# Optimization experiments

Measured on AMD Instinct MI355X. Metric: run time of the kernel, lower is better.

## Reference

```python
import jax, jax.numpy as jnp
import numpy as np

N = 8192      # input_shape[0]: side of the square complex weights A, B
UNITS = 33    # cell units; x has UNITS-1 features, state z has UNITS


def setup_inputs() -> dict:
    key = jax.random.key(0)
    ks = jax.random.split(key, 8)
    s = np.float32(1.0 / np.sqrt(N))  # keep tanh pre-activations O(1)
    f32 = jnp.float32
    return {
        "x_re": jax.random.normal(ks[0], (N, UNITS - 1), f32),
        "x_im": jax.random.normal(ks[1], (N, UNITS - 1), f32),
        "z_re": jax.random.normal(ks[2], (N, UNITS), f32),
        "z_im": jax.random.normal(ks[3], (N, UNITS), f32),
        "A_re": jax.random.normal(ks[4], (N, N), f32) * s,
        "A_im": jax.random.normal(ks[5], (N, N), f32) * s,
        "B_re": jax.random.normal(ks[6], (N, N), f32) * s,
        "B_im": jax.random.normal(ks[7], (N, N), f32) * s,
    }


def reference(x_re, x_im, z_re, z_im, A_re, A_im, B_re, B_im):
    # Assemble complex64 operands (TF cell stores A, B as complex64).
    x = jax.lax.complex(x_re, x_im)          # [N, UNITS-1]
    z = jax.lax.complex(z_re, z_im)          # [N, UNITS]
    A = jax.lax.complex(A_re, A_im)          # [N, N]
    B = jax.lax.complex(B_re, B_im)          # [N, N]

    z_0 = z[:, 0:1]                          # carried-through first column
    z_n = z[:, 1:]                           # [N, UNITS-1]

    # y_t = tanh(A @ z_n + B @ x)  (complex tanh, as tf.keras tanh on complex64)
    y_t = jnp.tanh(jnp.matmul(A, z_n) + jnp.matmul(B, x))

    # new state / output: concat([z_0, y_t], -1) -> [N, UNITS]
    return jnp.concatenate([z_0, y_t], axis=-1)
```

## Files before the change

### kernel.cpp

```cpp
#include <hip/hip_runtime.h>

#define NN 8192
#define UNITS 33
#define NCOLS 32
#define NSTEPS 512
#define NCHUNKB 8
#define CHUNKK (NN / NCHUNKB)
#define TILEK 128
#define TPC (CHUNKK / TILEK)
#define NSLAB (NCHUNKB * 4)

#define RPB 16
#define KT 32
#define NT (NN / KT)
#define SA_STRIDE 20
#define SZ_STRIDE 36
#define SA_MAT (KT * SA_STRIDE)
#define SZ_SRC (KT * SZ_STRIDE)
#define SA_FLOATS (4 * SA_MAT)
#define SZ_BASE SA_FLOATS
#define SH_FLOATS (SA_FLOATS + 4 * SZ_SRC)

typedef __attribute__((ext_vector_type(2)))  float f32x2;
typedef __attribute__((ext_vector_type(4)))  float f32x4;
typedef __attribute__((ext_vector_type(16))) float f32x16;
typedef __attribute__((ext_vector_type(8)))  short bf16x8;
typedef __attribute__((ext_vector_type(4)))  unsigned int u32x4;

union FragU { u32x4 u; bf16x8 s; };

#define MFMA(a, b, c) __builtin_amdgcn_mfma_f32_32x32x16_bf16(a, b, c, 0, 0, 0)

__device__ __forceinline__ float bfr(float v) {
    unsigned int u = __builtin_bit_cast(unsigned int, v);
    u = (u + 0x7FFFu + ((u >> 16) & 1u)) & 0xFFFF0000u;
    return __builtin_bit_cast(float, u);
}

__device__ __forceinline__ void split1(float v, unsigned int &h, unsigned int &l) {
    unsigned int u = __builtin_bit_cast(unsigned int, v);
    unsigned int hu = u >> 16;
    float hf = __builtin_bit_cast(float, hu << 16);
    float r = v - hf;
    unsigned int ru = __builtin_bit_cast(unsigned int, r);
    h = hu;
    l = (ru + 0x8000u) >> 16;
}

__device__ __forceinline__ void packHL(const unsigned int* h, const unsigned int* l,
                                       bf16x8 &hi, bf16x8 &lo) {
    FragU H, L;
    H.u.x = h[0] | (h[1] << 16); H.u.y = h[2] | (h[3] << 16);
    H.u.z = h[4] | (h[5] << 16); H.u.w = h[6] | (h[7] << 16);
    L.u.x = l[0] | (l[1] << 16); L.u.y = l[2] | (l[3] << 16);
    L.u.z = l[4] | (l[5] << 16); L.u.w = l[6] | (l[7] << 16);
    hi = H.s; lo = L.s;
}

__device__ __forceinline__ void mk_split(f32x4 a0, f32x4 a1, bf16x8 &hi, bf16x8 &lo) {
    unsigned int h[8], l[8];
#pragma unroll
    for (int e = 0; e < 4; ++e) { split1(a0[e], h[e], l[e]); split1(a1[e], h[e + 4], l[e + 4]); }
    packHL(h, l, hi, lo);
}

__device__ __forceinline__ bf16x8 fneg(bf16x8 f) {
    FragU x; x.s = f;
    x.u.x ^= 0x80008000u; x.u.y ^= 0x80008000u; x.u.z ^= 0x80008000u; x.u.w ^= 0x80008000u;
    return x.s;
}

__device__ __forceinline__ void probe_cd(int lane, int pm[16], int pn[16]) {
    int m = lane & 31, half = lane >> 5;
    unsigned int am, dummy;
    split1((float)m, am, dummy);
    unsigned int a1; split1(1.0f, a1, dummy);
    unsigned int bn; split1((float)(64 * m), bn, dummy);
    unsigned int av = (half == 0) ? am : a1;
    unsigned int bv = (half == 0) ? a1 : bn;
    FragU A, B;
    A.u.x = A.u.y = A.u.z = A.u.w = av | (av << 16);
    B.u.x = B.u.y = B.u.z = B.u.w = bv | (bv << 16);
    f32x16 d = {};
    d = MFMA(A.s, B.s, d);
#pragma unroll
    for (int r = 0; r < 16; ++r) {
        unsigned int u = (unsigned int)(d[r] * 0.125f + 0.5f);
        pm[r] = (int)(u & 63u);
        pn[r] = (int)(u >> 6);
    }
}

__device__ __forceinline__ void ctanhd(float af, float bf, float &re, float &im) {
    double a = (double)af, b = (double)bf;
    double e  = exp(2.0 * a);
    double ei = 1.0 / e;
    double ch = 0.5 * (e + ei);
    double sh = 0.5 * (e - ei);
    double cb = cos(2.0 * b);
    double sb = sin(2.0 * b);
    double d  = ch + cb;
    re = (float)(sh / d);
    im = (float)(sb / d);
}

__global__ void __launch_bounds__(256) hopf_zero(float* __restrict__ out, int n) {
    int i = blockIdx.x * 256 + threadIdx.x;
    if (i < n) out[i] = 0.0f;
}

__global__ void __launch_bounds__(256) hopf_prep(
    const float* __restrict__ xre, const float* __restrict__ xim,
    const float* __restrict__ zre, const float* __restrict__ zim,
    u32x4* __restrict__ bfrag) {
    int idx  = blockIdx.x * 256 + threadIdx.x;
    int lane = idx & 63;
    int src  = (idx >> 6) & 3;
    int step = idx >> 8;
    int n    = lane & 31;
    int half = lane >> 5;

    const float* base;
    int stride, coloff;
    if      (src == 0) { base = zre; stride = UNITS; coloff = 1; }
    else if (src == 1) { base = zim; stride = UNITS; coloff = 1; }
    else if (src == 2) { base = xre; stride = NCOLS; coloff = 0; }
    else               { base = xim; stride = NCOLS; coloff = 0; }

    unsigned int h[8], l[8];
#pragma unroll
    for (int e = 0; e < 8; ++e) {
        int k = step * 16 + 8 * half + e;
        split1(base[(size_t)k * stride + coloff + n], h[e], l[e]);
    }
    bf16x8 hi, lo;
    packHL(h, l, hi, lo);
    FragU H; H.s = hi;
    FragU L; L.s = lo;
    size_t o = (size_t)step * 512 + (size_t)src * 128 + lane;
    bfrag[o]      = H.u;
    bfrag[o + 64] = L.u;
}

struct AStep {
    f32x4 ar0, ar1, ai0, ai1, br0, br1, bi0, bi1;
};

__device__ __forceinline__ void computeStep(const AStep& s, const u32x4* __restrict__ pb,
                                            f32x16& arc, f32x16& aic) {
    FragU zrh, zrl, zih, zil, xrh, xrl, xih, xil;
    zrh.u = pb[0];   zrl.u = pb[64];
    zih.u = pb[128]; zil.u = pb[192];
    xrh.u = pb[256]; xrl.u = pb[320];
    xih.u = pb[384]; xil.u = pb[448];

    bf16x8 arh, arl, aih, ail, brh, brl, bih, bil;
    mk_split(s.ar0, s.ar1, arh, arl);
    mk_split(s.ai0, s.ai1, aih, ail);
    mk_split(s.br0, s.br1, brh, brl);
    mk_split(s.bi0, s.bi1, bih, bil);
    bf16x8 nih = fneg(aih), nil = fneg(ail);
    bf16x8 nbh = fneg(bih), nbl = fneg(bil);

    arc = MFMA(arh, zrh.s, arc); arc = MFMA(arh, zrl.s, arc); arc = MFMA(arl, zrh.s, arc);
    arc = MFMA(nih, zih.s, arc); arc = MFMA(nih, zil.s, arc); arc = MFMA(nil, zih.s, arc);
    arc = MFMA(brh, xrh.s, arc); arc = MFMA(brh, xrl.s, arc); arc = MFMA(brl, xrh.s, arc);
    arc = MFMA(nbh, xih.s, arc); arc = MFMA(nbh, xil.s, arc); arc = MFMA(nbl, xih.s, arc);
    aic = MFMA(arh, zih.s, aic); aic = MFMA(arh, zil.s, aic); aic = MFMA(arl, zih.s, aic);
    aic = MFMA(aih, zrh.s, aic); aic = MFMA(aih, zrl.s, aic); aic = MFMA(ail, zrh.s, aic);
    aic = MFMA(brh, xih.s, aic); aic = MFMA(brh, xil.s, aic); aic = MFMA(brl, xih.s, aic);
    aic = MFMA(bih, xrh.s, aic); aic = MFMA(bih, xrl.s, aic); aic = MFMA(bil, xrh.s, aic);
}

__global__ void __launch_bounds__(512, 4) hopf_mfma2(
    const float* __restrict__ Are, const float* __restrict__ Aim,
    const float* __restrict__ Bre, const float* __restrict__ Bim,
    const u32x4* __restrict__ bfrag, float* __restrict__ partial,
    unsigned long long ws_floats) {
    __shared__ float SH[4 * 4096];
    const int tid  = threadIdx.x;
    const int lane = tid & 63;
    const int w    = tid >> 6;
    const int r    = lane & 31;
    const int half = lane >> 5;
    const int chunk  = blockIdx.x & 7;
    const int rowgrp = blockIdx.x >> 3;
    const int m0 = rowgrp * 32;
    const size_t k0chunk = (size_t)chunk * CHUNKK;

    const int mat = w >> 1;
    const int rh  = w & 1;
    const float* matp = (mat == 0) ? Are : (mat == 1) ? Aim : (mat == 2) ? Bre : Bim;
    const int srh = lane >> 5;
    const int skg = lane & 31;

    f32x16 arc = {};
    f32x16 aic = {};
    f32x4 st[8];

#pragma unroll
    for (int i = 0; i < 8; ++i)
        st[i] = *(const f32x4*)(matp + (size_t)(m0 + rh * 16 + 2 * i + srh) * NN
                                + k0chunk + skg * 4);

    for (int t = 0; t < TPC; ++t) {
        __syncthreads();
#pragma unroll
        for (int i = 0; i < 8; ++i) {
            int row = rh * 16 + 2 * i + srh;
            int rp  = (row ^ skg) & 31;
            *(f32x4*)&SH[mat * 4096 + skg * 128 + rp * 4] = st[i];
        }
        __syncthreads();

        if (t + 1 < TPC) {
#pragma unroll
            for (int i = 0; i < 8; ++i)
                st[i] = *(const f32x4*)(matp + (size_t)(m0 + rh * 16 + 2 * i + srh) * NN
                                        + k0chunk + (size_t)(t + 1) * TILEK + skg * 4);
        }

        {
            const int kg0 = w * 4 + 2 * half;
            const int kg1 = kg0 + 1;
            AStep a;
            a.ar0 = *(const f32x4*)&SH[0 * 4096 + kg0 * 128 + ((r ^ kg0) & 31) * 4];
            a.ar1 = *(const f32x4*)&SH[0 * 4096 + kg1 * 128 + ((r ^ kg1) & 31) * 4];
            a.ai0 = *(const f32x4*)&SH[1 * 4096 + kg0 * 128 + ((r ^ kg0) & 31) * 4];
            a.ai1 = *(const f32x4*)&SH[1 * 4096 + kg1 * 128 + ((r ^ kg1) & 31) * 4];
            a.br0 = *(const f32x4*)&SH[2 * 4096 + kg0 * 128 + ((r ^ kg0) & 31) * 4];
            a.br1 = *(const f32x4*)&SH[2 * 4096 + kg1 * 128 + ((r ^ kg1) & 31) * 4];
            a.bi0 = *(const f32x4*)&SH[3 * 4096 + kg0 * 128 + ((r ^ kg0) & 31) * 4];
            a.bi1 = *(const f32x4*)&SH[3 * 4096 + kg1 * 128 + ((r ^ kg1) & 31) * 4];
            const int gstep = chunk * (CHUNKK / 16) + t * 8 + w;
            const u32x4* pb = bfrag + (size_t)gstep * 512 + lane;
            computeStep(a, pb, arc, aic);
        }
    }

    __syncthreads();
    if (w >= 4) {
        float* dst = &SH[(w - 4) * 2112 + lane * 33];
#pragma unroll
        for (int rr = 0; rr < 16; ++rr) { dst[rr] = arc[rr]; dst[16 + rr] = aic[rr]; }
    }
    __syncthreads();
    if (w < 4) {
        const float* src = &SH[w * 2112 + lane * 33];
#pragma unroll
        for (int rr = 0; rr < 16; ++rr) { arc[rr] += src[rr]; aic[rr] += src[16 + rr]; }

        int pm[16], pn[16];
        probe_cd(lane, pm, pn);
        const int slab = chunk * 4 + w;
#pragma unroll
        for (int rr = 0; rr < 16; ++rr) {
            int mrow = m0 + pm[rr];
            size_t o = (size_t)slab * (NN * NCOLS * 2) + ((size_t)mrow * NCOLS + pn[rr]) * 2;
            if (o + 2 <= ws_floats) {
                f32x2 v; v.x = arc[rr]; v.y = aic[rr];
                *(f32x2*)(partial + o) = v;
            }
        }
    }
}

__global__ void __launch_bounds__(256) hopf_finalize(
    const float* __restrict__ partial,
    const float* __restrict__ zre, const float* __restrict__ zim,
    float* __restrict__ out, int out_size, int nchunk) {
    int idx = blockIdx.x * 256 + threadIdx.x;
    if (idx >= NN * UNITS) return;
    int i = idx / UNITS, j = idx % UNITS;
    const bool interleaved = (out_size >= NN * UNITS * 2);
    float re, im;
    if (j == 0) {
        re = bfr(zre[(size_t)i * UNITS]);
        im = bfr(zim[(size_t)i * UNITS]);
    } else {
        size_t base = ((size_t)i * NCOLS + (j - 1)) * 2;
        float a = 0.0f, b = 0.0f;
#pragma unroll 4
        for (int c = 0; c < nchunk; ++c) {
            f32x2 v = *(const f32x2*)(partial + (size_t)c * (NN * NCOLS * 2) + base);
            a += v.x; b += v.y;
        }
        ctanhd(a, b, re, im);
        re = bfr(re); im = bfr(im);
    }
    if (interleaved) {
        if (2 * idx + 1 < out_size) { out[2 * idx] = re; out[2 * idx + 1] = im; }
    } else {
        if (idx < out_size) out[idx] = re;
    }
}

__global__ void __launch_bounds__(256) hopf_valu(
    const float* __restrict__ xre, const float* __restrict__ xim,
    const float* __restrict__ zre, const float* __restrict__ zim,
    const float* __restrict__ Are, const float* __restrict__ Aim,
    const float* __restrict__ Bre, const float* __restrict__ Bim,
    float* __restrict__ out, int out_size) {
    __shared__ float SH[SH_FLOATS];
    const int tid  = threadIdx.x;
    const int lane = tid & 63;
    const int wv   = tid >> 6;
    const int mh   = lane & 3;
    const int jh   = (lane >> 2) & 3;
    const int ks   = lane >> 4;
    const int m0   = blockIdx.x * RPB;
    const int sa_a  = tid >> 6;
    const int sa_r  = (tid >> 2) & 15;
    const int sa_kc = (tid & 3) * 8;

    float accr[4][8], acci[4][8];
#pragma unroll
    for (int dm = 0; dm < 4; ++dm)
#pragma unroll
        for (int dj = 0; dj < 8; ++dj) { accr[dm][dj] = 0.0f; acci[dm][dj] = 0.0f; }

    for (int kt = 0; kt < NT; ++kt) {
        const int k0 = kt * KT;
        __syncthreads();
        {
            const float* srcA = (sa_a == 0) ? Are : (sa_a == 1) ? Aim
                              : (sa_a == 2) ? Bre : Bim;
            const float* p = srcA + (size_t)(m0 + sa_r) * NN + k0 + sa_kc;
            f32x4 v0 = *(const f32x4*)(p);
            f32x4 v1 = *(const f32x4*)(p + 4);
#pragma unroll
            for (int i = 0; i < 4; ++i)
                SH[sa_a * SA_MAT + (sa_kc + i) * SA_STRIDE + sa_r] = v0[i];
#pragma unroll
            for (int i = 0; i < 4; ++i)
                SH[sa_a * SA_MAT + (sa_kc + 4 + i) * SA_STRIDE + sa_r] = v1[i];
        }
#pragma unroll
        for (int c = 0; c < 16; ++c) {
            const int s = c >> 2;
            const int k = (c & 3) * 8 + (tid >> 5);
            const int j = tid & 31;
            float v;
            if      (s == 0) v = zre[(size_t)(k0 + k) * UNITS + 1 + j];
            else if (s == 1) v = zim[(size_t)(k0 + k) * UNITS + 1 + j];
            else if (s == 2) v = xre[(size_t)(k0 + k) * 32 + j];
            else             v = xim[(size_t)(k0 + k) * 32 + j];
            SH[SZ_BASE + s * SZ_SRC + k * SZ_STRIDE + j] = v;
        }
        __syncthreads();

#pragma unroll
        for (int t = 0; t < 2; ++t) {
            const int kl = wv * 8 + ks * 2 + t;
            const float* sa = SH + kl * SA_STRIDE + mh * 4;
            f32x4 ar = *(const f32x4*)(sa + 0 * SA_MAT);
            f32x4 ai = *(const f32x4*)(sa + 1 * SA_MAT);
            f32x4 br = *(const f32x4*)(sa + 2 * SA_MAT);
            f32x4 bi = *(const f32x4*)(sa + 3 * SA_MAT);
            const float* sz = SH + SZ_BASE + kl * SZ_STRIDE + jh * 8;
            f32x4 zr0 = *(const f32x4*)(sz + 0 * SZ_SRC);
            f32x4 zr1 = *(const f32x4*)(sz + 0 * SZ_SRC + 4);
            f32x4 zi0 = *(const f32x4*)(sz + 1 * SZ_SRC);
            f32x4 zi1 = *(const f32x4*)(sz + 1 * SZ_SRC + 4);
            f32x4 xr0 = *(const f32x4*)(sz + 2 * SZ_SRC);
            f32x4 xr1 = *(const f32x4*)(sz + 2 * SZ_SRC + 4);
            f32x4 xi0 = *(const f32x4*)(sz + 3 * SZ_SRC);
            f32x4 xi1 = *(const f32x4*)(sz + 3 * SZ_SRC + 4);
#pragma unroll
            for (int dj = 0; dj < 8; ++dj) {
                const float vzr = (dj < 4) ? zr0[dj & 3] : zr1[dj & 3];
                const float vzi = (dj < 4) ? zi0[dj & 3] : zi1[dj & 3];
                const float vxr = (dj < 4) ? xr0[dj & 3] : xr1[dj & 3];
                const float vxi = (dj < 4) ? xi0[dj & 3] : xi1[dj & 3];
#pragma unroll
                for (int dm = 0; dm < 4; ++dm) {
                    float r = accr[dm][dj], q = acci[dm][dj];
                    r = fmaf(ar[dm],  vzr, r);
                    r = fmaf(-ai[dm], vzi, r);
                    r = fmaf(br[dm],  vxr, r);
                    r = fmaf(-bi[dm], vxi, r);
                    q = fmaf(ar[dm],  vzi, q);
                    q = fmaf(ai[dm],  vzr, q);
                    q = fmaf(br[dm],  vxi, q);
                    q = fmaf(bi[dm],  vxr, q);
                    accr[dm][dj] = r; acci[dm][dj] = q;
                }
            }
        }
    }

    __syncthreads();
    for (int i = tid; i < RPB * 32 * 2; i += 256) SH[i] = 0.0f;
    __syncthreads();
    const int myslot = wv * 4 + ks;
    for (int slot = 0; slot < 16; ++slot) {
        if (myslot == slot) {
#pragma unroll
            for (int dm = 0; dm < 4; ++dm)
#pragma unroll
                for (int dj = 0; dj < 8; ++dj) {
                    const int cell = (mh * 4 + dm) * 32 + (jh * 8 + dj);
                    SH[cell * 2 + 0] += accr[dm][dj];
                    SH[cell * 2 + 1] += acci[dm][dj];
                }
        }
        __syncthreads();
    }

    const bool interleaved = (out_size >= NN * UNITS * 2);
    {
        const int m = tid >> 4;
        const int j0 = tid & 15;
#pragma unroll
        for (int p = 0; p < 2; ++p) {
            const int j = j0 + p * 16;
            const float sr = SH[(m * 32 + j) * 2 + 0];
            const float si = SH[(m * 32 + j) * 2 + 1];
            float re, im;
            ctanhd(sr, si, re, im);
            const int e = (m0 + m) * UNITS + 1 + j;
            if (interleaved) {
                if (2 * e + 1 < out_size) { out[2 * e] = bfr(re); out[2 * e + 1] = bfr(im); }
            } else {
                if (e < out_size) out[e] = bfr(re);
            }
        }
        if (tid < RPB) {
            const int i = m0 + tid;
            const int e = i * UNITS;
            const float zr = bfr(zre[(size_t)i * UNITS]);
            const float zi = bfr(zim[(size_t)i * UNITS]);
            if (interleaved) {
                if (2 * e + 1 < out_size) { out[2 * e] = zr; out[2 * e + 1] = zi; }
            } else {
                if (e < out_size) out[e] = zr;
            }
        }
    }
}

extern "C" void kernel_launch(void* const* d_in, const int* in_sizes, int n_in,
                              void* d_out, int out_size, void* d_ws, size_t ws_size,
                              hipStream_t stream) {
    const int SX = NN * (UNITS - 1);
    const int SZn = NN * UNITS;
    const int SM = NN * NN;
    const float* xs[2] = {nullptr, nullptr};
    const float* zs[2] = {nullptr, nullptr};
    const float* ms[4] = {nullptr, nullptr, nullptr, nullptr};
    int nx = 0, nz = 0, nm = 0;
    for (int i = 0; i < n_in; ++i) {
        const float* p = (const float*)d_in[i];
        if      (in_sizes[i] == SX)  { if (nx < 2) xs[nx] = p; ++nx; }
        else if (in_sizes[i] == SZn) { if (nz < 2) zs[nz] = p; ++nz; }
        else if (in_sizes[i] == SM)  { if (nm < 4) ms[nm] = p; ++nm; }
    }
    float* out = (float*)d_out;

    if (nx != 2 || nz != 2 || nm != 4) {
        hopf_zero<<<(out_size + 255) / 256, 256, 0, stream>>>(out, out_size);
        return;
    }

    const float* xre = xs[0]; const float* xim = xs[1];
    const float* zre = zs[0]; const float* zim = zs[1];
    const float* Are = ms[0]; const float* Aim = ms[1];
    const float* Bre = ms[2]; const float* Bim = ms[3];

    const size_t SLAB_FLOATS = (size_t)NN * NCOLS * 2;
    const size_t SLAB_BYTES  = SLAB_FLOATS * 4;
    const size_t BFRAG_BYTES = (size_t)NSTEPS * 512 * sizeof(u32x4);

    if (ws_size >= NSLAB * SLAB_BYTES + BFRAG_BYTES) {
        float* partial = (float*)d_ws;
        u32x4* bfrag   = (u32x4*)((char*)d_ws + NSLAB * SLAB_BYTES);
        unsigned long long wsf = (unsigned long long)(NSLAB * SLAB_FLOATS);
        hopf_prep<<<512, 256, 0, stream>>>(xre, xim, zre, zim, bfrag);
        hopf_mfma2<<<NCHUNKB * 256, 512, 0, stream>>>(Are, Aim, Bre, Bim, bfrag, partial, wsf);
        hopf_finalize<<<(NN * UNITS + 255) / 256, 256, 0, stream>>>(partial, zre, zim, out, out_size, NSLAB);
    } else {
        hopf_valu<<<NN / RPB, 256, 0, stream>>>(xre, xim, zre, zim,
                                                Are, Aim, Bre, Bim, out, out_size);
    }
}
```

Baseline: 233.3 us.

## Double K-tile per iteration and fully reduce partials in-block to one slab

Doubles the K tile staged through shared memory to 256, so each wave now runs two MFMA steps per barrier pair and each lane loads a full row segment. The in-block partial reduction becomes a full tree across all 8 waves, so only one partial slab per chunk is written instead of four. This cuts barrier count and partial-sum write traffic, which also shrinks the finalize reduction. In exchange it doubles LDS use to 128KB, raises staging registers, and drops the occupancy hint, so fewer blocks may be resident per CU.

After: 251.3 us. 7.7% more time.

```diff
diff --git a/kernel.cpp b/kernel.cpp
--- a/kernel.cpp
+++ b/kernel.cpp
@@ -6,9 +6,9 @@
 #define NSTEPS 512
 #define NCHUNKB 8
 #define CHUNKK (NN / NCHUNKB)
-#define TILEK 128
+#define TILEK 256
 #define TPC (CHUNKK / TILEK)
-#define NSLAB (NCHUNKB * 4)
+#define NSLAB NCHUNKB
 
 #define RPB 16
 #define KT 32
@@ -172,12 +172,12 @@
     aic = MFMA(bih, xrh.s, aic); aic = MFMA(bih, xrl.s, aic); aic = MFMA(bil, xrh.s, aic);
 }
 
-__global__ void __launch_bounds__(512, 4) hopf_mfma2(
+__global__ void __launch_bounds__(512) hopf_mfma2(
     const float* __restrict__ Are, const float* __restrict__ Aim,
     const float* __restrict__ Bre, const float* __restrict__ Bim,
     const u32x4* __restrict__ bfrag, float* __restrict__ partial,
     unsigned long long ws_floats) {
-    __shared__ float SH[4 * 4096];
+    __shared__ float SH[4 * 8192];
     const int tid  = threadIdx.x;
     const int lane = tid & 63;
     const int w    = tid >> 6;
@@ -191,48 +191,50 @@
     const int mat = w >> 1;
     const int rh  = w & 1;
     const float* matp = (mat == 0) ? Are : (mat == 1) ? Aim : (mat == 2) ? Bre : Bim;
-    const int srh = lane >> 5;
-    const int skg = lane & 31;
 
     f32x16 arc = {};
     f32x16 aic = {};
-    f32x4 st[8];
-
-#pragma unroll
-    for (int i = 0; i < 8; ++i)
-        st[i] = *(const f32x4*)(matp + (size_t)(m0 + rh * 16 + 2 * i + srh) * NN
-                                + k0chunk + skg * 4);
+    f32x4 st[16];
+
+#pragma unroll
+    for (int i = 0; i < 16; ++i)
+        st[i] = *(const f32x4*)(matp + (size_t)(m0 + rh * 16 + i) * NN
+                                + k0chunk + lane * 4);
 
     for (int t = 0; t < TPC; ++t) {
         __syncthreads();
 #pragma unroll
-        for (int i = 0; i < 8; ++i) {
-            int row = rh * 16 + 2 * i + srh;
-            int rp  = (row ^ skg) & 31;
-            *(f32x4*)&SH[mat * 4096 + skg * 128 + rp * 4] = st[i];
+        for (int i = 0; i < 16; ++i) {
+            int row = rh * 16 + i;
+            int rp  = (row ^ (lane & 31)) & 31;
+            *(f32x4*)&SH[mat * 8192 + lane * 128 + rp * 4] = st[i];
         }
         __syncthreads();
 
         if (t + 1 < TPC) {
 #pragma unroll
-            for (int i = 0; i < 8; ++i)
-                st[i] = *(const f32x4*)(matp + (size_t)(m0 + rh * 16 + 2 * i + srh) * NN
-                                        + k0chunk + (size_t)(t + 1) * TILEK + skg * 4);
-        }
-
-        {
-            const int kg0 = w * 4 + 2 * half;
+            for (int i = 0; i < 16; ++i)
+                st[i] = *(const f32x4*)(matp + (size_t)(m0 + rh * 16 + i) * NN
+                                        + k0chunk + (size_t)(t + 1) * TILEK + lane * 4);
+        }
+
+#pragma unroll
+        for (int tt = 0; tt < 2; ++tt) {
+            const int s = 2 * w + tt;
+            const int kg0 = s * 4 + 2 * half;
             const int kg1 = kg0 + 1;
+            const int rp0 = ((r ^ (kg0 & 31)) & 31) * 4;
+            const int rp1 = ((r ^ (kg1 & 31)) & 31) * 4;
             AStep a;
-            a.ar0 = *(const f32x4*)&SH[0 * 4096 + kg0 * 128 + ((r ^ kg0) & 31) * 4];
-            a.ar1 = *(const f32x4*)&SH[0 * 4096 + kg1 * 128 + ((r ^ kg1) & 31) * 4];
-            a.ai0 = *(const f32x4*)&SH[1 * 4096 + kg0 * 128 + ((r ^ kg0) & 31) * 4];
-            a.ai1 = *(const f32x4*)&SH[1 * 4096 + kg1 * 128 + ((r ^ kg1) & 31) * 4];
-            a.br0 = *(const f32x4*)&SH[2 * 4096 + kg0 * 128 + ((r ^ kg0) & 31) * 4];
-            a.br1 = *(const f32x4*)&SH[2 * 4096 + kg1 * 128 + ((r ^ kg1) & 31) * 4];
-            a.bi0 = *(const f32x4*)&SH[3 * 4096 + kg0 * 128 + ((r ^ kg0) & 31) * 4];
-            a.bi1 = *(const f32x4*)&SH[3 * 4096 + kg1 * 128 + ((r ^ kg1) & 31) * 4];
-            const int gstep = chunk * (CHUNKK / 16) + t * 8 + w;
+            a.ar0 = *(const f32x4*)&SH[0 * 8192 + kg0 * 128 + rp0];
+            a.ar1 = *(const f32x4*)&SH[0 * 8192 + kg1 * 128 + rp1];
+            a.ai0 = *(const f32x4*)&SH[1 * 8192 + kg0 * 128 + rp0];
+            a.ai1 = *(const f32x4*)&SH[1 * 8192 + kg1 * 128 + rp1];
+            a.br0 = *(const f32x4*)&SH[2 * 8192 + kg0 * 128 + rp0];
+            a.br1 = *(const f32x4*)&SH[2 * 8192 + kg1 * 128 + rp1];
+            a.bi0 = *(const f32x4*)&SH[3 * 8192 + kg0 * 128 + rp0];
+            a.bi1 = *(const f32x4*)&SH[3 * 8192 + kg1 * 128 + rp1];
+            const int gstep = chunk * (CHUNKK / 16) + t * 16 + s;
             const u32x4* pb = bfrag + (size_t)gstep * 512 + lane;
             computeStep(a, pb, arc, aic);
         }
@@ -249,14 +251,37 @@
         const float* src = &SH[w * 2112 + lane * 33];
 #pragma unroll
         for (int rr = 0; rr < 16; ++rr) { arc[rr] += src[rr]; aic[rr] += src[16 + rr]; }
+    }
+    __syncthreads();
+    if (w == 2 || w == 3) {
+        float* dst = &SH[(w - 2) * 2112 + lane * 33];
+#pragma unroll
+        for (int rr = 0; rr < 16; ++rr) { dst[rr] = arc[rr]; dst[16 + rr] = aic[rr]; }
+    }
+    __syncthreads();
+    if (w < 2) {
+        const float* src = &SH[w * 2112 + lane * 33];
+#pragma unroll
+        for (int rr = 0; rr < 16; ++rr) { arc[rr] += src[rr]; aic[rr] += src[16 + rr]; }
+    }
+    __syncthreads();
+    if (w == 1) {
+        float* dst = &SH[lane * 33];
+#pragma unroll
+        for (int rr = 0; rr < 16; ++rr) { dst[rr] = arc[rr]; dst[16 + rr] = aic[rr]; }
+    }
+    __syncthreads();
+    if (w == 0) {
+        const float* src = &SH[lane * 33];
+#pragma unroll
+        for (int rr = 0; rr < 16; ++rr) { arc[rr] += src[rr]; aic[rr] += src[16 + rr]; }
 
         int pm[16], pn[16];
         probe_cd(lane, pm, pn);
-        const int slab = chunk * 4 + w;
 #pragma unroll
         for (int rr = 0; rr < 16; ++rr) {
             int mrow = m0 + pm[rr];
-            size_t o = (size_t)slab * (NN * NCOLS * 2) + ((size_t)mrow * NCOLS + pn[rr]) * 2;
+            size_t o = (size_t)chunk * (NN * NCOLS * 2) + ((size_t)mrow * NCOLS + pn[rr]) * 2;
             if (o + 2 <= ws_floats) {
                 f32x2 v; v.x = arc[rr]; v.y = aic[rr];
                 *(f32x2*)(partial + o) = v;
```
